# Kernel optimization log

Hardware: AMD Instinct MI355X
Metric: run time of the kernel (lower is better)

The kernel has to match this reference:

```python
import jax, jax.numpy as jnp
import numpy as np

B, N, F_IN, D = 32768, 4, 512, 64  # N fixed to 4 by the max_pool(4,1)+reshape


def setup_inputs() -> dict:
    key = jax.random.key(0)
    k1, k2, k3, k4 = jax.random.split(key, 4)
    scale = 1.0 / np.sqrt(F_IN)
    return {
        "drug": jax.random.normal(k1, (B, N, F_IN), dtype=jnp.float32),
        "Wk": jax.random.normal(k2, (F_IN, D), dtype=jnp.float32) * scale,
        "Wq": jax.random.normal(k3, (F_IN, D), dtype=jnp.float32) * scale,
        "Wv": jax.random.normal(k4, (F_IN, D), dtype=jnp.float32) * scale,
    }


def reference(drug, Wk, Wq, Wv):
    # projections: torch nn.Linear(bias=False) -> x @ W  (W stored as [in, out] here)
    k = jnp.einsum("bnf,fd->bnd", drug, Wk)
    q = jnp.einsum("bnf,fd->bnd", drug, Wq)
    v = jnp.einsum("bnf,fd->bnd", drug, Wv)
    # score = bmm(K, Q^T); NOTE: no 1/sqrt(d) scaling, matching the source
    score = jnp.einsum("bnd,bmd->bnm", k, q)  # [B, N, N]
    attn = jax.nn.softmax(score, axis=2)
    out = jnp.einsum("bnm,bmd->bnd", attn, v)  # [B, N, D]
    # max_pool2d kernel (4,1), stride (4,1) over N=4 -> max over axis 1, then reshape [B, D]
    return jnp.max(out, axis=1)
```

## Files before the change

### kernel.cpp

```cpp
#include <hip/hip_runtime.h>
#include <hip/hip_fp16.h>

#define BTOT   32768
#define FIN    512
#define NCOLS  192
#define KSTEPS 16
#define NTILES 12
#define WH_ELEMS (KSTEPS * NTILES * 64 * 8)
#define CHUNK_HALVES (NTILES * 64 * 8)
#define CHUNK_BYTES  (CHUNK_HALVES * 2)
#define PHASES 8

using half8   = __attribute__((ext_vector_type(8))) _Float16;
using floatx4 = __attribute__((ext_vector_type(4))) float;

#define GLOAD_LDS16(gp, lp)                                                  \
    __builtin_amdgcn_global_load_lds(                                        \
        (const __attribute__((address_space(1))) void*)(gp),                 \
        (__attribute__((address_space(3))) void*)(lp), 16, 0, 0)

__global__ void convert_w_kernel(const float* __restrict__ Wk,
                                 const float* __restrict__ Wq,
                                 const float* __restrict__ Wv,
                                 _Float16* __restrict__ Wh) {
    int idx = blockIdx.x * blockDim.x + threadIdx.x;
    if (idx >= WH_ELEMS) return;
    int j    = idx & 7;
    int lane = (idx >> 3) & 63;
    int t    = (idx >> 9) % NTILES;
    int kk   = idx / CHUNK_HALVES;
    int k = kk * 32 + (lane >> 4) * 8 + j;
    int n = t * 16 + (lane & 15);
    const float* src = (n < 64) ? Wk : (n < 128) ? Wq : Wv;
    Wh[idx] = (_Float16)src[k * 64 + (n & 63)];
}

__global__ __launch_bounds__(256) void attn_fused_kernel(
        const float* __restrict__ drug,
        const _Float16* __restrict__ Wh,
        float* __restrict__ out)
{
    __shared__ __align__(16) char lds[2 * CHUNK_BYTES];

    const int tid  = threadIdx.x;
    const int wave = tid >> 6;
    const int lane = tid & 63;
    const int quad = lane >> 4;
    const int l15  = lane & 15;

    const int row = blockIdx.x * 64 + wave * 16 + l15;
    const float* arow = drug + (size_t)row * FIN + quad * 8;
    const char* gW = (const char*)Wh;

    floatx4 acc[NTILES];
#pragma unroll
    for (int t = 0; t < NTILES; ++t) acc[t] = (floatx4){0.f, 0.f, 0.f, 0.f};

    for (int ph = 0; ph < PHASES; ++ph) {
        __syncthreads();

        const size_t goff = (size_t)ph * 2 * CHUNK_BYTES;
#pragma unroll
        for (int i = 0; i < 6; ++i) {
            const int off = i * 4096 + wave * 1024;
            GLOAD_LDS16(gW + goff + off + lane * 16, lds + off);
        }

        const float4* ap0 = (const float4*)(arow + (2 * ph) * 32);
        const float4* ap1 = (const float4*)(arow + (2 * ph + 1) * 32);
        float4 a00 = ap0[0], a01 = ap0[1];
        float4 a10 = ap1[0], a11 = ap1[1];

        half8 afrag[2];
        afrag[0][0] = (_Float16)a00.x; afrag[0][1] = (_Float16)a00.y;
        afrag[0][2] = (_Float16)a00.z; afrag[0][3] = (_Float16)a00.w;
        afrag[0][4] = (_Float16)a01.x; afrag[0][5] = (_Float16)a01.y;
        afrag[0][6] = (_Float16)a01.z; afrag[0][7] = (_Float16)a01.w;
        afrag[1][0] = (_Float16)a10.x; afrag[1][1] = (_Float16)a10.y;
        afrag[1][2] = (_Float16)a10.z; afrag[1][3] = (_Float16)a10.w;
        afrag[1][4] = (_Float16)a11.x; afrag[1][5] = (_Float16)a11.y;
        afrag[1][6] = (_Float16)a11.z; afrag[1][7] = (_Float16)a11.w;

        __syncthreads();

#pragma unroll
        for (int s = 0; s < 2; ++s) {
            const _Float16* lh = (const _Float16*)(lds + s * CHUNK_BYTES);
#pragma unroll
            for (int t = 0; t < NTILES; ++t) {
                half8 bfrag = *((const half8*)(lh + (t * 64 + lane) * 8));
                acc[t] = __builtin_amdgcn_mfma_f32_16x16x32_f16(afrag[s], bfrag, acc[t], 0, 0, 0);
            }
        }
    }

    float p[4][4];
#pragma unroll
    for (int n = 0; n < 4; ++n)
#pragma unroll
        for (int m = 0; m < 4; ++m) {
            float s = 0.f;
#pragma unroll
            for (int t = 0; t < 4; ++t) s += acc[t][n] * acc[4 + t][m];
            p[n][m] = s;
        }

#pragma unroll
    for (int mask = 1; mask < 16; mask <<= 1) {
#pragma unroll
        for (int n = 0; n < 4; ++n)
#pragma unroll
            for (int m = 0; m < 4; ++m)
                p[n][m] += __shfl_xor(p[n][m], mask, 64);
    }

    float res[4] = {-INFINITY, -INFINITY, -INFINITY, -INFINITY};
#pragma unroll
    for (int n = 0; n < 4; ++n) {
        float mx = fmaxf(fmaxf(p[n][0], p[n][1]), fmaxf(p[n][2], p[n][3]));
        float e0 = __expf(p[n][0] - mx);
        float e1 = __expf(p[n][1] - mx);
        float e2 = __expf(p[n][2] - mx);
        float e3 = __expf(p[n][3] - mx);
        float inv = 1.f / (e0 + e1 + e2 + e3);
#pragma unroll
        for (int t = 0; t < 4; ++t) {
            float o = (e0 * acc[8 + t][0] + e1 * acc[8 + t][1] +
                       e2 * acc[8 + t][2] + e3 * acc[8 + t][3]) * inv;
            res[t] = fmaxf(res[t], o);
        }
    }

    const int b = blockIdx.x * 16 + wave * 4 + quad;
#pragma unroll
    for (int t = 0; t < 4; ++t)
        out[b * 64 + t * 16 + l15] = res[t];
}

extern "C" void kernel_launch(void* const* d_in, const int* in_sizes, int n_in,
                              void* d_out, int out_size, void* d_ws, size_t ws_size,
                              hipStream_t stream) {
    const float* drug = (const float*)d_in[0];
    const float* Wk   = (const float*)d_in[1];
    const float* Wq   = (const float*)d_in[2];
    const float* Wv   = (const float*)d_in[3];
    float* out = (float*)d_out;
    _Float16* Wh = (_Float16*)d_ws;

    convert_w_kernel<<<(WH_ELEMS + 255) / 256, 256, 0, stream>>>(Wk, Wq, Wv, Wh);
    attn_fused_kernel<<<BTOT / 16, 256, 0, stream>>>(drug, Wh, out);
}
```

Baseline: 368.3 us.

## Read weight fragments directly from global memory and prefetch next activation slice

Removes the LDS staging of the fp16 weight chunks and both per-phase block barriers, so each wave loads its B fragments straight from global memory, relying on L1/L2 caching of the small shared weight buffer. The activation loads for the next k-step are issued one iteration ahead as a software prefetch to hide global latency. This trades barrier and LDS traffic for more global/cache load instructions per wave, with redundant weight fetches across the four waves.

```diff
diff --git a/kernel.cpp b/kernel.cpp
--- a/kernel.cpp
+++ b/kernel.cpp
@@ -8,16 +8,9 @@
 #define NTILES 12
 #define WH_ELEMS (KSTEPS * NTILES * 64 * 8)
 #define CHUNK_HALVES (NTILES * 64 * 8)
-#define CHUNK_BYTES  (CHUNK_HALVES * 2)
-#define PHASES 8
 
 using half8   = __attribute__((ext_vector_type(8))) _Float16;
 using floatx4 = __attribute__((ext_vector_type(4))) float;
-
-#define GLOAD_LDS16(gp, lp)                                                  \
-    __builtin_amdgcn_global_load_lds(                                        \
-        (const __attribute__((address_space(1))) void*)(gp),                 \
-        (__attribute__((address_space(3))) void*)(lp), 16, 0, 0)
 
 __global__ void convert_w_kernel(const float* __restrict__ Wk,
                                  const float* __restrict__ Wq,
@@ -40,8 +33,6 @@
         const _Float16* __restrict__ Wh,
         float* __restrict__ out)
 {
-    __shared__ __align__(16) char lds[2 * CHUNK_BYTES];
-
     const int tid  = threadIdx.x;
     const int wave = tid >> 6;
     const int lane = tid & 63;
@@ -50,49 +41,40 @@
 
     const int row = blockIdx.x * 64 + wave * 16 + l15;
     const float* arow = drug + (size_t)row * FIN + quad * 8;
-    const char* gW = (const char*)Wh;
+    const half8* wf = (const half8*)Wh + lane;
 
     floatx4 acc[NTILES];
 #pragma unroll
     for (int t = 0; t < NTILES; ++t) acc[t] = (floatx4){0.f, 0.f, 0.f, 0.f};
 
-    for (int ph = 0; ph < PHASES; ++ph) {
-        __syncthreads();
+    float4 a0 = ((const float4*)arow)[0];
+    float4 a1 = ((const float4*)arow)[1];
 
-        const size_t goff = (size_t)ph * 2 * CHUNK_BYTES;
-#pragma unroll
-        for (int i = 0; i < 6; ++i) {
-            const int off = i * 4096 + wave * 1024;
-            GLOAD_LDS16(gW + goff + off + lane * 16, lds + off);
-        }
+#define KSTEP_BODY(KKI)                                                       \
+    do {                                                                      \
+        half8 af;                                                             \
+        af[0] = (_Float16)a0.x; af[1] = (_Float16)a0.y;                       \
+        af[2] = (_Float16)a0.z; af[3] = (_Float16)a0.w;                       \
+        af[4] = (_Float16)a1.x; af[5] = (_Float16)a1.y;                       \
+        af[6] = (_Float16)a1.z; af[7] = (_Float16)a1.w;                       \
+        const half8* bp = wf + (KKI) * (NTILES * 64);                         \
+        _Pragma("unroll")                                                     \
+        for (int t = 0; t < NTILES; ++t) {                                    \
+            half8 bf = bp[t * 64];                                            \
+            acc[t] = __builtin_amdgcn_mfma_f32_16x16x32_f16(af, bf, acc[t], 0, 0, 0); \
+        }                                                                     \
+    } while (0)
 
-        const float4* ap0 = (const float4*)(arow + (2 * ph) * 32);
-        const float4* ap1 = (const float4*)(arow + (2 * ph + 1) * 32);
-        float4 a00 = ap0[0], a01 = ap0[1];
-        float4 a10 = ap1[0], a11 = ap1[1];
-
-        half8 afrag[2];
-        afrag[0][0] = (_Float16)a00.x; afrag[0][1] = (_Float16)a00.y;
-        afrag[0][2] = (_Float16)a00.z; afrag[0][3] = (_Float16)a00.w;
-        afrag[0][4] = (_Float16)a01.x; afrag[0][5] = (_Float16)a01.y;
-        afrag[0][6] = (_Float16)a01.z; afrag[0][7] = (_Float16)a01.w;
-        afrag[1][0] = (_Float16)a10.x; afrag[1][1] = (_Float16)a10.y;
-        afrag[1][2] = (_Float16)a10.z; afrag[1][3] = (_Float16)a10.w;
-        afrag[1][4] = (_Float16)a11.x; afrag[1][5] = (_Float16)a11.y;
-        afrag[1][6] = (_Float16)a11.z; afrag[1][7] = (_Float16)a11.w;
-
-        __syncthreads();
-
-#pragma unroll
-        for (int s = 0; s < 2; ++s) {
-            const _Float16* lh = (const _Float16*)(lds + s * CHUNK_BYTES);
-#pragma unroll
-            for (int t = 0; t < NTILES; ++t) {
-                half8 bfrag = *((const half8*)(lh + (t * 64 + lane) * 8));
-                acc[t] = __builtin_amdgcn_mfma_f32_16x16x32_f16(afrag[s], bfrag, acc[t], 0, 0, 0);
-            }
-        }
+#pragma unroll 1
+    for (int kk = 0; kk < KSTEPS - 1; ++kk) {
+        const float4* ap = (const float4*)(arow + (kk + 1) * 32);
+        float4 n0 = ap[0];
+        float4 n1 = ap[1];
+        KSTEP_BODY(kk);
+        a0 = n0; a1 = n1;
     }
+    KSTEP_BODY(KSTEPS - 1);
+#undef KSTEP_BODY
 
     float p[4][4];
 #pragma unroll
```

Result: slower. 419.4 us (+13.9%).

## Double-buffer weight chunks in LDS with vmcnt-based software pipelining

Applied to the files above, without the earlier changes.

Replaces the phase loop, which loaded two weight chunks and then synchronized, with a per-k-step double-buffered pipeline. The next chunk is prefetched into the alternate LDS buffer via global_load_lds while the MFMAs run on the current one, using explicit s_waitcnt vmcnt and s_barrier. The activation row for step k+1 is register-prefetched during step k. The aim is to hide the latency of weight and activation loads behind compute. In exchange there are twice as many barriers per chunk. The hand-counted vmcnt also depends on the compiler's ordering of the global loads, which is fragile.

```diff
diff --git a/kernel.cpp b/kernel.cpp
--- a/kernel.cpp
+++ b/kernel.cpp
@@ -9,7 +9,6 @@
 #define WH_ELEMS (KSTEPS * NTILES * 64 * 8)
 #define CHUNK_HALVES (NTILES * 64 * 8)
 #define CHUNK_BYTES  (CHUNK_HALVES * 2)
-#define PHASES 8
 
 using half8   = __attribute__((ext_vector_type(8))) _Float16;
 using floatx4 = __attribute__((ext_vector_type(4))) float;
@@ -56,43 +55,61 @@
 #pragma unroll
     for (int t = 0; t < NTILES; ++t) acc[t] = (floatx4){0.f, 0.f, 0.f, 0.f};
 
-    for (int ph = 0; ph < PHASES; ++ph) {
-        __syncthreads();
+#define STAGE(K)                                                             \
+    do {                                                                     \
+        const char* _s = gW + (size_t)(K) * CHUNK_BYTES;                     \
+        char* _d = lds + ((K) & 1) * CHUNK_BYTES;                            \
+        _Pragma("unroll")                                                    \
+        for (int _i = 0; _i < 3; ++_i) {                                     \
+            const int _off = (wave + 4 * _i) * 1024;                         \
+            GLOAD_LDS16(_s + _off + lane * 16, _d + _off);                   \
+        }                                                                    \
+    } while (0)
 
-        const size_t goff = (size_t)ph * 2 * CHUNK_BYTES;
+    STAGE(0);
+    float4 a0 = ((const float4*)arow)[0];
+    float4 a1 = ((const float4*)arow)[1];
+    STAGE(1);
+
 #pragma unroll
-        for (int i = 0; i < 6; ++i) {
-            const int off = i * 4096 + wave * 1024;
-            GLOAD_LDS16(gW + goff + off + lane * 16, lds + off);
+    for (int k = 0; k < KSTEPS; ++k) {
+        if (k < KSTEPS - 1)
+            asm volatile("s_waitcnt vmcnt(3)" ::: "memory");
+        else
+            asm volatile("s_waitcnt vmcnt(0)" ::: "memory");
+        asm volatile("" ::: "memory");
+        __builtin_amdgcn_s_barrier();
+        asm volatile("" ::: "memory");
+
+        float4 n0, n1;
+        if (k < KSTEPS - 1) {
+            const float4* ap = (const float4*)(arow + (k + 1) * 32);
+            n0 = ap[0];
+            n1 = ap[1];
         }
 
-        const float4* ap0 = (const float4*)(arow + (2 * ph) * 32);
-        const float4* ap1 = (const float4*)(arow + (2 * ph + 1) * 32);
-        float4 a00 = ap0[0], a01 = ap0[1];
-        float4 a10 = ap1[0], a11 = ap1[1];
+        half8 af;
+        af[0] = (_Float16)a0.x; af[1] = (_Float16)a0.y;
+        af[2] = (_Float16)a0.z; af[3] = (_Float16)a0.w;
+        af[4] = (_Float16)a1.x; af[5] = (_Float16)a1.y;
+        af[6] = (_Float16)a1.z; af[7] = (_Float16)a1.w;
 
-        half8 afrag[2];
-        afrag[0][0] = (_Float16)a00.x; afrag[0][1] = (_Float16)a00.y;
-        afrag[0][2] = (_Float16)a00.z; afrag[0][3] = (_Float16)a00.w;
-        afrag[0][4] = (_Float16)a01.x; afrag[0][5] = (_Float16)a01.y;
-        afrag[0][6] = (_Float16)a01.z; afrag[0][7] = (_Float16)a01.w;
-        afrag[1][0] = (_Float16)a10.x; afrag[1][1] = (_Float16)a10.y;
-        afrag[1][2] = (_Float16)a10.z; afrag[1][3] = (_Float16)a10.w;
-        afrag[1][4] = (_Float16)a11.x; afrag[1][5] = (_Float16)a11.y;
-        afrag[1][6] = (_Float16)a11.z; afrag[1][7] = (_Float16)a11.w;
+        const _Float16* lh = (const _Float16*)(lds + (k & 1) * CHUNK_BYTES);
+#pragma unroll
+        for (int t = 0; t < NTILES; ++t) {
+            half8 bf = *((const half8*)(lh + (t * 64 + lane) * 8));
+            acc[t] = __builtin_amdgcn_mfma_f32_16x16x32_f16(af, bf, acc[t], 0, 0, 0);
+        }
 
-        __syncthreads();
-
-#pragma unroll
-        for (int s = 0; s < 2; ++s) {
-            const _Float16* lh = (const _Float16*)(lds + s * CHUNK_BYTES);
-#pragma unroll
-            for (int t = 0; t < NTILES; ++t) {
-                half8 bfrag = *((const half8*)(lh + (t * 64 + lane) * 8));
-                acc[t] = __builtin_amdgcn_mfma_f32_16x16x32_f16(afrag[s], bfrag, acc[t], 0, 0, 0);
-            }
+        if (k < KSTEPS - 2) {
+            asm volatile("" ::: "memory");
+            __builtin_amdgcn_s_barrier();
+            asm volatile("" ::: "memory");
+            STAGE(k + 2);
         }
+        a0 = n0; a1 = n1;
     }
+#undef STAGE
 
     float p[4][4];
 #pragma unroll
```

Measured after the change: 372.0 us. No clear change (+1.0%).
